# Optimization experiments

Measured on AMD Instinct MI355X. Metric: run time of the kernel, lower is better.

The kernel has to match this reference:

```python
import jax, jax.numpy as jnp
import numpy as np

H = 8          # SD1.4 heads
TAU = 0.1      # HarmCfg.tau
GAMMA = 1.0    # HarmCfg.gamma
EPS = 1e-12    # F.normalize eps


def setup_inputs() -> dict:
    key = jax.random.key(0)
    ks = jax.random.split(key, 8)
    B, S, C, K, D = 16, 4096, 320, 77, 768
    return {
        "hidden_states": jax.random.normal(ks[0], (B, S, C), jnp.float32),
        "encoder_hidden_states": jax.random.normal(ks[1], (B, K, D), jnp.float32),
        "harm_vec": jax.random.normal(ks[2], (D,), jnp.float32),
        "Wq": jax.random.normal(ks[3], (C, C), jnp.float32) * 0.02,
        "Wk": jax.random.normal(ks[4], (D, C), jnp.float32) * 0.02,
        "Wv": jax.random.normal(ks[5], (D, C), jnp.float32) * 0.02,
        "Wo": jax.random.normal(ks[6], (C, C), jnp.float32) * 0.02,
        "bo": jnp.zeros((C,), jnp.float32),
    }


def reference(hidden_states, encoder_hidden_states, harm_vec, Wq, Wk, Wv, Wo, bo):
    B, S, C = hidden_states.shape
    K = encoder_hidden_states.shape[1]
    dh = C // H
    scale = 1.0 / jnp.sqrt(jnp.asarray(dh, hidden_states.dtype))

    # projections (no bias on q/k/v, as in diffusers SD1.4)
    q = (hidden_states @ Wq).reshape(B, S, H, dh)
    k = (encoder_hidden_states @ Wk).reshape(B, K, H, dh)
    v = (encoder_hidden_states @ Wv).reshape(B, K, H, dh)

    # scores: QK^T / sqrt(dh)  -> [B, H, S, K]
    scores = jnp.einsum('bqhd,bkhd->bhqk', q, k) * scale

    # cosine-similarity harmful-token penalty (broadcast over heads and queries)
    harm = harm_vec / jnp.maximum(jnp.linalg.norm(harm_vec), EPS)
    ctx_norm = encoder_hidden_states / jnp.maximum(
        jnp.linalg.norm(encoder_hidden_states, axis=-1, keepdims=True), EPS)
    cos = jnp.einsum('bkd,d->bk', ctx_norm, harm)            # [B, K]
    penalty = jnp.maximum(cos - TAU, 0.0)                     # clamp(min=0)
    scores = scores - GAMMA * penalty[:, None, None, :]

    probs = jax.nn.softmax(scores, axis=-1)                   # dropout p=0 (eval)
    out = jnp.einsum('bhqk,bkhd->bqhd', probs, v).reshape(B, S, C)
    return out @ Wo + bo
```

## Files before the change

kernel.cpp:

```cpp
#include <hip/hip_runtime.h>
#include <hip/hip_bf16.h>

#define B_ 16
#define S_ 4096
#define C_ 320
#define KK_ 77
#define D_ 768
#define H_ 8
#define DH_ 40
#define KP_ 80
#define NP_ (H_ * KP_)
#define TAU_ 0.1f
#define GAMMA_ 1.0f
#define EPS_ 1e-12f

typedef __bf16 bf16x8 __attribute__((ext_vector_type(8)));
typedef float f32x4 __attribute__((ext_vector_type(4)));
typedef unsigned short ushort8v __attribute__((ext_vector_type(8)));
typedef unsigned int u32;

__device__ __forceinline__ unsigned short f2bf(float f) {
    union { float f; unsigned u; } v; v.f = f;
    unsigned r = v.u + 0x7fffu + ((v.u >> 16) & 1u);
    return (unsigned short)(r >> 16);
}

__device__ __forceinline__ void gld16(const unsigned short* g, char* l) {
    __builtin_amdgcn_global_load_lds(
        (const __attribute__((address_space(1))) u32*)g,
        (__attribute__((address_space(3))) u32*)l, 16, 0, 0);
}

__global__ __launch_bounds__(256) void build_M(const float* __restrict__ Wq,
        const float* __restrict__ Wk, const float* __restrict__ Wv,
        const float* __restrict__ Wo, unsigned short* __restrict__ Bmat) {
    const int Dk = blockIdx.x * 256 + threadIdx.x;
    const int h = blockIdx.y;
    const int which = blockIdx.z >> 2;
    const int c0 = (blockIdx.z & 3) * 80;
    __shared__ float wlds[80 * 44];
    for (int i = threadIdx.x; i < 80 * DH_; i += 256) {
        int c = i / DH_, d = i % DH_;
        wlds[c * 44 + d] = which
            ? Wo[(size_t)(h * DH_ + d) * C_ + (c0 + c)]
            : Wq[(size_t)(c0 + c) * C_ + h * DH_ + d];
    }
    float a[DH_];
    const float* Arow = (which ? Wv : Wk) + (size_t)Dk * C_ + h * DH_;
    #pragma unroll
    for (int d = 0; d < DH_; ++d) a[d] = Arow[d];
    __syncthreads();
    const float scale = 0.15811388300841898f;
    for (int c = 0; c < 80; ++c) {
        float s = 0.f;
        #pragma unroll
        for (int q = 0; q < 10; ++q) {
            float4 wv4 = *(const float4*)&wlds[c * 44 + q * 4];
            s += a[q * 4 + 0] * wv4.x + a[q * 4 + 1] * wv4.y
               + a[q * 4 + 2] * wv4.z + a[q * 4 + 3] * wv4.w;
        }
        if (!which) s *= scale;
        int n = which * 2560 + h * C_ + c0 + c;
        Bmat[(size_t)n * D_ + Dk] = f2bf(s);
    }
}

__global__ __launch_bounds__(256) void prep_ehs(const float* __restrict__ ehs,
        const float* __restrict__ harm, unsigned short* __restrict__ ehs_bf,
        float* __restrict__ pen) {
    const int w = threadIdx.x >> 6, l = threadIdx.x & 63;
    const int kk = blockIdx.x * 4 + w, b = blockIdx.y;
    const size_t obase = ((size_t)b * KP_ + kk) * D_;
    if (kk >= KK_) {
        #pragma unroll
        for (int j = 0; j < 12; ++j) ehs_bf[obase + l + j * 64] = 0;
        if (l == 0) pen[b * KP_ + kk] = 0.f;
        return;
    }
    const float* er = ehs + ((size_t)b * KK_ + kk) * D_;
    float ss = 0.f, dd = 0.f, hh = 0.f;
    #pragma unroll
    for (int j = 0; j < 12; ++j) {
        float e = er[l + j * 64], hv = harm[l + j * 64];
        ehs_bf[obase + l + j * 64] = f2bf(e);
        ss += e * e; dd += e * hv; hh += hv * hv;
    }
    #pragma unroll
    for (int off = 32; off; off >>= 1) {
        ss += __shfl_xor(ss, off);
        dd += __shfl_xor(dd, off);
        hh += __shfl_xor(hh, off);
    }
    if (l == 0) {
        float cs = dd / (fmaxf(sqrtf(ss), EPS_) * fmaxf(sqrtf(hh), EPS_));
        pen[b * KP_ + kk] = GAMMA_ * fmaxf(cs - TAU_, 0.f);
    }
}

__global__ __launch_bounds__(1024) void gemm_WpU(
        const unsigned short* __restrict__ ehs_bf,
        const unsigned short* __restrict__ Bmat,
        unsigned short* __restrict__ Wp, unsigned short* __restrict__ U) {
    const int id = blockIdx.x;
    const int b = id & 15, nt = id >> 4;
    const int tid = threadIdx.x, w = tid >> 6, l = tid & 63;
    const int lrow = l & 15, lgrp = l >> 4, lk = lgrp * 8;
    __shared__ unsigned short Al[80 * 768];
    char* lds = (char*)Al;

    const unsigned short* Ag = ehs_bf + (size_t)b * KP_ * D_;
    #pragma unroll
    for (int it = 0; it < 8; ++it) {
        int ch = tid + it * 1024;
        if (ch < 7680) {
            int byte = ch * 16, row = byte / 1536;
            int a = byte ^ ((row & 7) << 4);
            *(ushort8v*)(lds + a) = *(const ushort8v*)(Ag + ch * 8);
        }
    }
    const int n0 = nt * 512 + w * 32;
    const unsigned short* Br = Bmat + (size_t)(n0 + lrow) * D_ + lk;
    bf16x8 bC[2], bN[2];
    #pragma unroll
    for (int nf = 0; nf < 2; ++nf)
        bC[nf] = *(const bf16x8*)(Br + (size_t)nf * 16 * D_);
    __syncthreads();

    f32x4 acc[5][2];
    #pragma unroll
    for (int mf = 0; mf < 5; ++mf)
        #pragma unroll
        for (int nf = 0; nf < 2; ++nf) acc[mf][nf] = (f32x4){0.f, 0.f, 0.f, 0.f};
    #pragma unroll
    for (int ks = 0; ks < D_ / 32; ++ks) {
        if (ks < D_ / 32 - 1) {
            #pragma unroll
            for (int nf = 0; nf < 2; ++nf)
                bN[nf] = *(const bf16x8*)(Br + (size_t)nf * 16 * D_ + (ks + 1) * 32);
        }
        bf16x8 af[5];
        #pragma unroll
        for (int mf = 0; mf < 5; ++mf) {
            int row = mf * 16 + lrow;
            int a = (row * 1536 + (ks * 32 + lk) * 2) ^ ((row & 7) << 4);
            af[mf] = *(const bf16x8*)(lds + a);
        }
        __builtin_amdgcn_s_setprio(1);
        #pragma unroll
        for (int mf = 0; mf < 5; ++mf)
            #pragma unroll
            for (int nf = 0; nf < 2; ++nf)
                acc[mf][nf] = __builtin_amdgcn_mfma_f32_16x16x32_bf16(
                    af[mf], bC[nf], acc[mf][nf], 0, 0, 0);
        __builtin_amdgcn_s_setprio(0);
        #pragma unroll
        for (int nf = 0; nf < 2; ++nf) bC[nf] = bN[nf];
    }
    #pragma unroll
    for (int nf = 0; nf < 2; ++nf) {
        const int col = n0 + nf * 16 + lrow;
        if (col < 2560) {
            const int h = col / C_, c = col % C_;
            #pragma unroll
            for (int mf = 0; mf < 5; ++mf)
                #pragma unroll
                for (int r = 0; r < 4; ++r) {
                    int kk = mf * 16 + lgrp * 4 + r;
                    Wp[((size_t)b * NP_ + h * KP_ + kk) * C_ + c] = f2bf(acc[mf][nf][r]);
                }
        } else {
            const int n2 = col - 2560;
            const int h = n2 / C_, c = n2 % C_;
            #pragma unroll
            for (int mf = 0; mf < 5; ++mf)
                #pragma unroll
                for (int r = 0; r < 4; ++r) {
                    int kk = mf * 16 + lgrp * 4 + r;
                    U[((size_t)b * C_ + c) * NP_ + h * KP_ + kk] = f2bf(acc[mf][nf][r]);
                }
        }
    }
}

__global__ __launch_bounds__(1024) void fused_attn(
        const float* __restrict__ hs, const unsigned short* __restrict__ Wp,
        const unsigned short* __restrict__ U, const float* __restrict__ pen,
        const float* __restrict__ bo, float* __restrict__ out) {
    const int id = blockIdx.x;
    const int xcd = id & 7, rest = id >> 3;
    const int b = xcd * 2 + (rest >> 6);
    const int s0 = (rest & 63) * 64;
    __shared__ __align__(16) char smem[122880];
    char* HS = smem;
    char* WB0 = smem + 40960;
    char* WB1 = smem + 81920;
    char* PB  = smem + 40960;
    char* UB0 = smem;
    char* UB1 = smem + 20480;
    const int tid = threadIdx.x, w = tid >> 6, l = tid & 63;
    const int lrow = l & 15, lgrp = l >> 4, lk = lgrp * 8;
    const int h = w & 7, mh = w >> 3;
    const int mgrp = w & 3, ngrp = w >> 2;

    const unsigned short* Wpb = Wp + (size_t)b * NP_ * C_;
    const unsigned short* Ub  = U  + (size_t)b * C_ * NP_;

    auto stage_wp = [&](int ks, char* buf) {
        #pragma unroll
        for (int j = 0; j < 2; ++j) {
            int L = w * 128 + j * 64 + l;
            int n = L >> 2, cs = (L & 3) ^ ((n >> 1) & 3);
            gld16(Wpb + (size_t)n * C_ + ks * 32 + cs * 8,
                  buf + (w * 128 + j * 64) * 16);
        }
        if (w < 8) {
            int L = 2048 + w * 64 + l;
            int n = L >> 2, cs = (L & 3) ^ ((n >> 1) & 3);
            gld16(Wpb + (size_t)n * C_ + ks * 32 + cs * 8,
                  buf + (2048 + w * 64) * 16);
        }
    };
    auto stage_u = [&](int ksn, char* buf) {
        {
            int L = w * 64 + l;
            int c = L >> 2, cs = (L & 3) ^ ((c >> 1) & 3);
            gld16(Ub + (size_t)c * NP_ + ksn * 32 + cs * 8, buf + (w * 64) * 16);
        }
        if (w < 4) {
            int L = 1024 + w * 64 + l;
            int c = L >> 2, cs = (L & 3) ^ ((c >> 1) & 3);
            gld16(Ub + (size_t)c * NP_ + ksn * 32 + cs * 8,
                  buf + (1024 + w * 64) * 16);
        }
    };

    stage_wp(0, WB0);
    const float4* hv = (const float4*)(hs + ((size_t)b * S_ + s0) * C_);
    #pragma unroll
    for (int it = 0; it < 5; ++it) {
        int i = tid + it * 1024;
        float4 v = hv[i];
        int r = i / 80, c = (i * 4) % C_;
        ushort4 u;
        u.x = f2bf(v.x); u.y = f2bf(v.y); u.z = f2bf(v.z); u.w = f2bf(v.w);
        int a = (r * 640 + c * 2) ^ ((r & 7) << 4);
        *(ushort4*)(HS + a) = u;
    }
    float4 pv4[5];
    #pragma unroll
    for (int nf = 0; nf < 5; ++nf)
        pv4[nf] = *(const float4*)(pen + b * KP_ + nf * 16 + lgrp * 4);
    __syncthreads();

    f32x4 acc[5][2];
    #pragma unroll
    for (int nf = 0; nf < 5; ++nf)
        #pragma unroll
        for (int mf = 0; mf < 2; ++mf) acc[nf][mf] = (f32x4){0.f, 0.f, 0.f, 0.f};
    for (int ks = 0; ks < 10; ++ks) {
        if (ks < 9) stage_wp(ks + 1, (ks & 1) ? WB0 : WB1);
        char* wb = (ks & 1) ? WB1 : WB0;
        bf16x8 bC[5], hf[2];
        #pragma unroll
        for (int nf = 0; nf < 5; ++nf) {
            int n = h * KP_ + nf * 16 + lrow;
            bC[nf] = *(const bf16x8*)(wb + n * 64 + ((lgrp ^ ((n >> 1) & 3)) << 4));
        }
        #pragma unroll
        for (int mf = 0; mf < 2; ++mf) {
            int row = mh * 32 + mf * 16 + lrow;
            int a = (row * 640 + (ks * 32 + lk) * 2) ^ ((row & 7) << 4);
            hf[mf] = *(const bf16x8*)(HS + a);
        }
        __builtin_amdgcn_s_setprio(1);
        #pragma unroll
        for (int nf = 0; nf < 5; ++nf)
            #pragma unroll
            for (int mf = 0; mf < 2; ++mf)
                acc[nf][mf] = __builtin_amdgcn_mfma_f32_16x16x32_bf16(
                    bC[nf], hf[mf], acc[nf][mf], 0, 0, 0);
        __builtin_amdgcn_s_setprio(0);
        __syncthreads();
    }

    stage_u(0, UB0);

    float inv2[2];
    #pragma unroll
    for (int mf = 0; mf < 2; ++mf) {
        float mx = -1e30f;
        #pragma unroll
        for (int nf = 0; nf < 5; ++nf)
            #pragma unroll
            for (int r = 0; r < 4; ++r) {
                float x = acc[nf][mf][r] - ((const float*)&pv4[nf])[r];
                if (nf == 4 && r >= 1) x = (lgrp == 3) ? -1e30f : x;
                acc[nf][mf][r] = x;
                mx = fmaxf(mx, x);
            }
        mx = fmaxf(mx, __shfl_xor(mx, 16));
        mx = fmaxf(mx, __shfl_xor(mx, 32));
        float s = 0.f;
        #pragma unroll
        for (int nf = 0; nf < 5; ++nf)
            #pragma unroll
            for (int r = 0; r < 4; ++r) {
                float e = __expf(acc[nf][mf][r] - mx);
                acc[nf][mf][r] = e; s += e;
            }
        s += __shfl_xor(s, 16);
        s += __shfl_xor(s, 32);
        inv2[mf] = 1.f / s;
    }

    #pragma unroll
    for (int mf = 0; mf < 2; ++mf) {
        const int m = mh * 32 + mf * 16 + lrow;
        const float inv = inv2[mf];
        #pragma unroll
        for (int nf = 0; nf < 5; ++nf) {
            ushort4 u;
            u.x = f2bf(acc[nf][mf][0] * inv);
            u.y = f2bf(acc[nf][mf][1] * inv);
            u.z = f2bf(acc[nf][mf][2] * inv);
            u.w = f2bf(acc[nf][mf][3] * inv);
            int a = (m * 1280 + (h * KP_ + nf * 16 + lgrp * 4) * 2) ^ ((m & 7) << 4);
            *(ushort4*)(PB + a) = u;
        }
    }
    __syncthreads();

    f32x4 acc2[5];
    #pragma unroll
    for (int nf = 0; nf < 5; ++nf) acc2[nf] = (f32x4){0.f, 0.f, 0.f, 0.f};
    float bov[5];
    #pragma unroll
    for (int nf = 0; nf < 5; ++nf) bov[nf] = bo[ngrp * KP_ + nf * 16 + lrow];
    for (int ksn = 0; ksn < 20; ++ksn) {
        if (ksn < 19) stage_u(ksn + 1, (ksn & 1) ? UB0 : UB1);
        char* ub = (ksn & 1) ? UB1 : UB0;
        bf16x8 pa, uf[5];
        {
            int row = mgrp * 16 + lrow;
            int a = (row * 1280 + (ksn * 32 + lk) * 2) ^ ((row & 7) << 4);
            pa = *(const bf16x8*)(PB + a);
        }
        #pragma unroll
        for (int nf = 0; nf < 5; ++nf) {
            int c = ngrp * KP_ + nf * 16 + lrow;
            uf[nf] = *(const bf16x8*)(ub + c * 64 + ((lgrp ^ ((c >> 1) & 3)) << 4));
        }
        __builtin_amdgcn_s_setprio(1);
        #pragma unroll
        for (int nf = 0; nf < 5; ++nf)
            acc2[nf] = __builtin_amdgcn_mfma_f32_16x16x32_bf16(pa, uf[nf], acc2[nf], 0, 0, 0);
        __builtin_amdgcn_s_setprio(0);
        __syncthreads();
    }
    float* op = out + ((size_t)b * S_ + s0) * C_;
    #pragma unroll
    for (int r = 0; r < 4; ++r)
        #pragma unroll
        for (int nf = 0; nf < 5; ++nf)
            op[(size_t)(mgrp * 16 + lgrp * 4 + r) * C_ +
               ngrp * KP_ + nf * 16 + lrow] = acc2[nf][r] + bov[nf];
}

extern "C" void kernel_launch(void* const* d_in, const int* in_sizes, int n_in,
                              void* d_out, int out_size, void* d_ws, size_t ws_size,
                              hipStream_t stream) {
    const float* hs   = (const float*)d_in[0];
    const float* ehs  = (const float*)d_in[1];
    const float* harm = (const float*)d_in[2];
    const float* Wq   = (const float*)d_in[3];
    const float* Wk   = (const float*)d_in[4];
    const float* Wv   = (const float*)d_in[5];
    const float* Wo   = (const float*)d_in[6];
    const float* bo   = (const float*)d_in[7];
    float* out = (float*)d_out;

    char* ws = (char*)d_ws;
    unsigned short* ehs_bf = (unsigned short*)(ws);
    unsigned short* Bmat   = (unsigned short*)(ws + 1966080);
    float*          pen    = (float*)        (ws + 9830400);
    unsigned short* Wp     = (unsigned short*)(ws + 9835520);
    unsigned short* U      = (unsigned short*)(ws + 16389120);

    build_M <<<dim3(3, 8, 8),  256, 0, stream>>>(Wq, Wk, Wv, Wo, Bmat);
    prep_ehs<<<dim3(20, 16),   256, 0, stream>>>(ehs, harm, ehs_bf, pen);
    gemm_WpU<<<dim3(160),     1024, 0, stream>>>(ehs_bf, Bmat, Wp, U);
    fused_attn<<<dim3(1024),  1024, 0, stream>>>(hs, Wp, U, pen, bo, out);
}
```

Before: 176.3 us.

## Deepen LDS staging pipeline with explicit vmcnt waits and split barriers

Stages two weight tiles ahead and issues the next global-to-LDS load right after the current tile's compute. Hand-placed s_waitcnt vmcnt counts let each wave wait only for the older tile, replacing the full __syncthreads that drained all outstanding loads. The k loops are fully unrolled, and the bias load moves after the second GEMM to cut register pressure. This adds a second barrier per iteration, and correctness now depends on the hand-tuned per-wave outstanding-load counts.

Result: no change. 175.4 us (-0.5%).

```diff
diff --git a/kernel.cpp b/kernel.cpp
--- a/kernel.cpp
+++ b/kernel.cpp
@@ -18,6 +18,11 @@
 typedef float f32x4 __attribute__((ext_vector_type(4)));
 typedef unsigned short ushort8v __attribute__((ext_vector_type(8)));
 typedef unsigned int u32;
+
+#define WAITV(N)  asm volatile("s_waitcnt vmcnt(" #N ")" ::: "memory")
+#define WAITVL(N) asm volatile("s_waitcnt vmcnt(" #N ") lgkmcnt(0)" ::: "memory")
+#define WAITLG()  asm volatile("s_waitcnt lgkmcnt(0)" ::: "memory")
+#define BAR()     __builtin_amdgcn_s_barrier()
 
 __device__ __forceinline__ unsigned short f2bf(float f) {
     union { float f; unsigned u; } v; v.f = f;
@@ -234,7 +239,10 @@
         }
     };
 
-    stage_wp(0, WB0);
+    float4 pv4[5];
+    #pragma unroll
+    for (int nf = 0; nf < 5; ++nf)
+        pv4[nf] = *(const float4*)(pen + b * KP_ + nf * 16 + lgrp * 4);
     const float4* hv = (const float4*)(hs + ((size_t)b * S_ + s0) * C_);
     #pragma unroll
     for (int it = 0; it < 5; ++it) {
@@ -246,19 +254,22 @@
         int a = (r * 640 + c * 2) ^ ((r & 7) << 4);
         *(ushort4*)(HS + a) = u;
     }
-    float4 pv4[5];
     #pragma unroll
     for (int nf = 0; nf < 5; ++nf)
-        pv4[nf] = *(const float4*)(pen + b * KP_ + nf * 16 + lgrp * 4);
-    __syncthreads();
+        asm volatile("" :: "v"(pv4[nf].x), "v"(pv4[nf].y),
+                           "v"(pv4[nf].z), "v"(pv4[nf].w));
+    stage_wp(0, WB0);
+    stage_wp(1, WB1);
+    if (w < 8) { WAITVL(3); } else { WAITVL(2); }
+    BAR();
 
     f32x4 acc[5][2];
     #pragma unroll
     for (int nf = 0; nf < 5; ++nf)
         #pragma unroll
         for (int mf = 0; mf < 2; ++mf) acc[nf][mf] = (f32x4){0.f, 0.f, 0.f, 0.f};
+    #pragma unroll
     for (int ks = 0; ks < 10; ++ks) {
-        if (ks < 9) stage_wp(ks + 1, (ks & 1) ? WB0 : WB1);
         char* wb = (ks & 1) ? WB1 : WB0;
         bf16x8 bC[5], hf[2];
         #pragma unroll
@@ -280,10 +291,21 @@
                 acc[nf][mf] = __builtin_amdgcn_mfma_f32_16x16x32_bf16(
                     bC[nf], hf[mf], acc[nf][mf], 0, 0, 0);
         __builtin_amdgcn_s_setprio(0);
-        __syncthreads();
+        WAITLG();
+        BAR();
+        if (ks < 9) {
+            if (ks < 8) {
+                stage_wp(ks + 2, wb);
+                if (w < 8) { WAITV(3); } else { WAITV(2); }
+            } else {
+                WAITV(0);
+            }
+            BAR();
+        }
     }
 
     stage_u(0, UB0);
+    stage_u(1, UB1);
 
     float inv2[2];
     #pragma unroll
@@ -328,16 +350,14 @@
             *(ushort4*)(PB + a) = u;
         }
     }
-    __syncthreads();
+    if (w < 4) { WAITVL(2); } else { WAITVL(1); }
+    BAR();
 
     f32x4 acc2[5];
     #pragma unroll
     for (int nf = 0; nf < 5; ++nf) acc2[nf] = (f32x4){0.f, 0.f, 0.f, 0.f};
-    float bov[5];
-    #pragma unroll
-    for (int nf = 0; nf < 5; ++nf) bov[nf] = bo[ngrp * KP_ + nf * 16 + lrow];
+    #pragma unroll
     for (int ksn = 0; ksn < 20; ++ksn) {
-        if (ksn < 19) stage_u(ksn + 1, (ksn & 1) ? UB0 : UB1);
         char* ub = (ksn & 1) ? UB1 : UB0;
         bf16x8 pa, uf[5];
         {
@@ -355,8 +375,21 @@
         for (int nf = 0; nf < 5; ++nf)
             acc2[nf] = __builtin_amdgcn_mfma_f32_16x16x32_bf16(pa, uf[nf], acc2[nf], 0, 0, 0);
         __builtin_amdgcn_s_setprio(0);
-        __syncthreads();
-    }
+        WAITLG();
+        BAR();
+        if (ksn < 19) {
+            if (ksn < 18) {
+                stage_u(ksn + 2, ub);
+                if (w < 4) { WAITV(2); } else { WAITV(1); }
+            } else {
+                WAITV(0);
+            }
+            BAR();
+        }
+    }
+    float bov[5];
+    #pragma unroll
+    for (int nf = 0; nf < 5; ++nf) bov[nf] = bo[ngrp * KP_ + nf * 16 + lrow];
     float* op = out + ((size_t)b * S_ + s0) * C_;
     #pragma unroll
     for (int r = 0; r < 4; ++r)
```
